# Kernel optimization log

Measured on AMD Instinct MI355X. Metric: run time of the kernel, lower is better.

The kernel has to match this reference:

```python
import jax, jax.numpy as jnp
import numpy as np

HIDDEN = 2048
NUM_Q_HEADS = 32
NUM_KV_HEADS = 8
HEAD_DIM = HIDDEN // NUM_Q_HEADS  # 64
GROUPS = NUM_Q_HEADS // NUM_KV_HEADS  # 4
MAX_WAVELENGTH = 10000.0
B, S = 2, 1024
NEG_INF = -1e9  # keras Softmax masking constant


def apply_rope(x, start_index=0, max_wavelength=MAX_WAVELENGTH):
    # x: [b, s, h, d]; keras_hub RotaryEmbedding (split-half / Llama style)
    d = x.shape[-1]
    s = x.shape[1]
    freq_range = jnp.arange(0, d, 2, dtype=jnp.float32)
    inverse_freq = 1.0 / (max_wavelength ** (freq_range / d))  # [d/2]
    positions = jnp.arange(s, dtype=jnp.float32) + start_index
    freq = positions[:, None] * inverse_freq[None, :]  # [s, d/2]
    emb = jnp.concatenate([freq, freq], axis=-1)[None, :, None, :]  # [1,s,1,d]
    cos = jnp.cos(emb).astype(x.dtype)
    sin = jnp.sin(emb).astype(x.dtype)
    x1, x2 = jnp.split(x, 2, axis=-1)
    half_rot = jnp.concatenate([-x2, x1], axis=-1)
    return x * cos + half_rot * sin


def setup_inputs() -> dict:
    key = jax.random.key(0)
    k1, k2, k3, k4, k5 = jax.random.split(key, 5)
    hidden_states = jax.random.normal(k1, (B, S, HIDDEN), dtype=jnp.float32)
    # causal mask, broadcast over batch
    attention_mask = jnp.broadcast_to(
        jnp.tril(jnp.ones((S, S), dtype=bool))[None], (B, S, S)
    )
    scale = 1.0 / np.sqrt(HIDDEN)
    Wq = jax.random.normal(k2, (HIDDEN, NUM_Q_HEADS * HEAD_DIM), dtype=jnp.float32) * scale
    Wk = jax.random.normal(k3, (HIDDEN, NUM_KV_HEADS * HEAD_DIM), dtype=jnp.float32) * scale
    Wv = jax.random.normal(k4, (HIDDEN, NUM_KV_HEADS * HEAD_DIM), dtype=jnp.float32) * scale
    Wo = jax.random.normal(k5, (NUM_Q_HEADS * HEAD_DIM, HIDDEN), dtype=jnp.float32) * scale
    return {"hidden_states": hidden_states, "attention_mask": attention_mask,
            "Wq": Wq, "Wk": Wk, "Wv": Wv, "Wo": Wo}


def reference(hidden_states, attention_mask, Wq, Wk, Wv, Wo):
    b, s, _ = hidden_states.shape
    q = (hidden_states @ Wq).reshape(b, s, NUM_Q_HEADS, HEAD_DIM)
    k = (hidden_states @ Wk).reshape(b, s, NUM_KV_HEADS, HEAD_DIM)
    v = (hidden_states @ Wv).reshape(b, s, NUM_KV_HEADS, HEAD_DIM)
    q = apply_rope(q)
    k = apply_rope(k)
    # GQA: repeat kv heads to match query heads (ops.repeat on axis 2)
    k = jnp.repeat(k, GROUPS, axis=2)
    v = jnp.repeat(v, GROUPS, axis=2)
    inv_norm = 1.0 / np.sqrt(HEAD_DIM)
    scores = jnp.einsum("bquh,bkuh->buqk", q, k) * inv_norm  # [b, h, q, k]
    scores = scores.astype(jnp.float32)
    scores = jnp.where(attention_mask[:, None, :, :], scores, NEG_INF)
    probs = jax.nn.softmax(scores, axis=-1).astype(hidden_states.dtype)
    attn = jnp.einsum("buqk,bkuh->bquh", probs, v)  # [b, q, h, hd]
    attn = attn.reshape(b, s, HIDDEN)
    return attn @ Wo
```

## Files before the change

### kernel.cpp

```cpp
#include <hip/hip_runtime.h>
#include <hip/hip_bf16.h>
#include <math.h>

#define S_LEN 1024
#define BATCH 2
#define HIDDEN 2048
#define NQH 32
#define NKVH 8
#define HD 64
#define LDQKV 3072
#define M_ROWS (BATCH * S_LEN)

typedef __attribute__((ext_vector_type(8))) short bf16x8;
typedef __attribute__((ext_vector_type(4))) float f32x4;

typedef unsigned int uint32_g __attribute__((address_space(1)));
typedef unsigned int uint32_l __attribute__((address_space(3)));

static __device__ __forceinline__ void load_lds16(const void* g, void* l) {
    __builtin_amdgcn_global_load_lds((const uint32_g*)g, (uint32_l*)l, 16, 0, 0);
}

static __device__ __forceinline__ short f2bf(float f) {
    union { __hip_bfloat16 h; short s; } cv;
    cv.h = __float2bfloat16(f);
    return cv.s;
}

__global__ __launch_bounds__(256) void conv_all_kernel(
    const float* __restrict__ X,
    const float* __restrict__ Wq, const float* __restrict__ Wk,
    const float* __restrict__ Wv, const float* __restrict__ Wo,
    short* __restrict__ Xb, short* __restrict__ Wqkvt, short* __restrict__ Wot,
    float2* __restrict__ cs2)
{
    __shared__ short Ts[64][68];
    const int tid = threadIdx.x;

    if (blockIdx.z == 4) {
        int flat = blockIdx.y * 32 + blockIdx.x;
        size_t base = (size_t)flat * 4096 + (size_t)tid * 16;
        #pragma unroll
        for (int rep = 0; rep < 2; ++rep) {
            size_t i = base + rep * 8;
            float4 a = *reinterpret_cast<const float4*>(X + i);
            float4 b = *reinterpret_cast<const float4*>(X + i + 4);
            union { bf16x8 v; short s[8]; } t;
            t.s[0] = f2bf(a.x); t.s[1] = f2bf(a.y); t.s[2] = f2bf(a.z); t.s[3] = f2bf(a.w);
            t.s[4] = f2bf(b.x); t.s[5] = f2bf(b.y); t.s[6] = f2bf(b.z); t.s[7] = f2bf(b.w);
            *reinterpret_cast<bf16x8*>(Xb + i) = t.v;
        }
        if (flat < 128) {
            int g = flat * 256 + tid;
            int s = g >> 5, i = g & 31;
            float inv_freq = 1.0f / powf(10000.0f, (float)i / 32.0f);
            float freq = (float)s * inv_freq;
            double sn, cs;
            sincos((double)freq, &sn, &cs);
            cs2[g] = make_float2((float)cs, (float)sn);
        }
        return;
    }

    const float* src; short* dst; int N;
    switch (blockIdx.z) {
        case 0: src = Wq; dst = Wqkvt;                         N = 2048; break;
        case 1: src = Wk; dst = Wqkvt + (size_t)2048 * 2048;   N = 512;  break;
        case 2: src = Wv; dst = Wqkvt + (size_t)2560 * 2048;   N = 512;  break;
        default: src = Wo; dst = Wot;                          N = 2048; break;
    }
    const int n0 = blockIdx.x * 64, k0 = blockIdx.y * 64;
    if (n0 >= N) return;

    #pragma unroll
    for (int rep = 0; rep < 4; ++rep) {
        int idx = rep * 256 + tid;
        int row = idx >> 4, c4 = (idx & 15) * 4;
        float4 v = *reinterpret_cast<const float4*>(
            src + (size_t)(k0 + row) * N + n0 + c4);
        ushort4 u;
        u.x = (unsigned short)f2bf(v.x); u.y = (unsigned short)f2bf(v.y);
        u.z = (unsigned short)f2bf(v.z); u.w = (unsigned short)f2bf(v.w);
        *reinterpret_cast<ushort4*>(&Ts[row][c4]) = u;
    }
    __syncthreads();
    #pragma unroll
    for (int rep = 0; rep < 2; ++rep) {
        int idx = rep * 256 + tid;
        int n = idx >> 3, kc = (idx & 7) * 8;
        union { bf16x8 v; short s[8]; } t;
        #pragma unroll
        for (int j = 0; j < 8; ++j) t.s[j] = Ts[kc + j][n];
        *reinterpret_cast<bf16x8*>(dst + (size_t)(n0 + n) * 2048 + k0 + kc) = t.v;
    }
}

template <bool ROPE_BF16>
__global__ __launch_bounds__(256) void gemm_bf16_kernel(
    const short* __restrict__ A, const short* __restrict__ Bt,
    float* __restrict__ C, short* __restrict__ Cb,
    short* __restrict__ vt_g,
    const float2* __restrict__ cs2, int K, int ldc)
{
    const int n0 = blockIdx.x * 64, m0 = blockIdx.y * 128;
    const int tid = threadIdx.x;
    const int w = tid >> 6, lane = tid & 63;
    const int m15 = lane & 15, q4 = lane >> 4;

    __shared__ short SL[128 * 64 + 64 * 64];
    short (*As)[64] = (short(*)[64])SL;
    short (*Bs)[64] = (short(*)[64])(SL + 128 * 64);

    f32x4 acc[2][4];
    #pragma unroll
    for (int i = 0; i < 2; ++i)
        #pragma unroll
        for (int j = 0; j < 4; ++j) acc[i][j] = (f32x4){0.f, 0.f, 0.f, 0.f};

    const int srow = lane >> 3;
    const int pchunk = lane & 7;

    for (int k0 = 0; k0 < K; k0 += 64) {
        __syncthreads();
        #pragma unroll
        for (int r = 0; r < 4; ++r) {
            int row = (w * 4 + r) * 8 + srow;
            int lchunk = pchunk ^ (row & 7);
            load_lds16(A + (size_t)(m0 + row) * K + k0 + lchunk * 8,
                       &As[(w * 4 + r) * 8][0]);
        }
        #pragma unroll
        for (int r = 0; r < 2; ++r) {
            int row = (w * 2 + r) * 8 + srow;
            int lchunk = pchunk ^ (row & 7);
            load_lds16(Bt + (size_t)(n0 + row) * K + k0 + lchunk * 8,
                       &Bs[(w * 2 + r) * 8][0]);
        }
        __syncthreads();

        #pragma unroll
        for (int ch = 0; ch < 2; ++ch) {
            bf16x8 af[2], bf[4];
            #pragma unroll
            for (int mt = 0; mt < 2; ++mt) {
                int row = w * 32 + mt * 16 + m15;
                af[mt] = *reinterpret_cast<const bf16x8*>(
                    &As[row][(((ch * 4 + q4) ^ (row & 7))) * 8]);
            }
            #pragma unroll
            for (int nt = 0; nt < 4; ++nt) {
                int row = nt * 16 + m15;
                bf[nt] = *reinterpret_cast<const bf16x8*>(
                    &Bs[row][(((ch * 4 + q4) ^ (row & 7))) * 8]);
            }
            #pragma unroll
            for (int mt = 0; mt < 2; ++mt)
                #pragma unroll
                for (int nt = 0; nt < 4; ++nt)
                    acc[mt][nt] = __builtin_amdgcn_mfma_f32_16x16x32_bf16(
                        af[mt], bf[nt], acc[mt][nt], 0, 0, 0);
        }
    }

    if (!ROPE_BF16) {
        #pragma unroll
        for (int mt = 0; mt < 2; ++mt)
            #pragma unroll
            for (int nt = 0; nt < 4; ++nt)
                #pragma unroll
                for (int reg = 0; reg < 4; ++reg)
                    C[(size_t)(m0 + w * 32 + mt * 16 + q4 * 4 + reg) * ldc
                      + n0 + nt * 16 + m15] = acc[mt][nt][reg];
    } else if (n0 < 2560) {
        #pragma unroll
        for (int mt = 0; mt < 2; ++mt) {
            #pragma unroll
            for (int reg = 0; reg < 4; ++reg) {
                int row = m0 + w * 32 + mt * 16 + q4 * 4 + reg;
                int s = row & (S_LEN - 1);
                float2 t0 = cs2[s * 32 + m15];
                float2 t1 = cs2[s * 32 + 16 + m15];
                float a0 = acc[mt][0][reg], a1 = acc[mt][1][reg];
                float a2 = acc[mt][2][reg], a3 = acc[mt][3][reg];
                size_t base = (size_t)row * ldc + n0 + m15;
                Cb[base +  0] = f2bf(a0 * t0.x - a2 * t0.y);
                Cb[base + 16] = f2bf(a1 * t1.x - a3 * t1.y);
                Cb[base + 32] = f2bf(a2 * t0.x + a0 * t0.y);
                Cb[base + 48] = f2bf(a3 * t1.x + a1 * t1.y);
            }
        }
    } else {
        __syncthreads();
        short (*VT)[136] = (short(*)[136])SL;
        #pragma unroll
        for (int mt = 0; mt < 2; ++mt) {
            #pragma unroll
            for (int nt = 0; nt < 4; ++nt) {
                ushort4 u;
                u.x = (unsigned short)f2bf(acc[mt][nt][0]);
                u.y = (unsigned short)f2bf(acc[mt][nt][1]);
                u.z = (unsigned short)f2bf(acc[mt][nt][2]);
                u.w = (unsigned short)f2bf(acc[mt][nt][3]);
                *reinterpret_cast<ushort4*>(
                    &VT[nt * 16 + m15][w * 32 + mt * 16 + q4 * 4]) = u;
            }
        }
        __syncthreads();
        const int kvh = (n0 - 2560) >> 6;
        const int b = m0 >> 10, k0loc = m0 & (S_LEN - 1);
        const int dim = tid >> 2, kc = (tid & 3) * 32;
        short* dst = vt_g + (size_t)((b * 8 + kvh) * 64 + dim) * S_LEN + k0loc + kc;
        #pragma unroll
        for (int u = 0; u < 4; ++u)
            *reinterpret_cast<bf16x8*>(dst + u * 8) =
                *reinterpret_cast<const bf16x8*>(&VT[dim][kc + u * 8]);
    }
}

__global__ __launch_bounds__(256) void attn_kernel(
    const short* __restrict__ qkvb, const short* __restrict__ vt_g,
    short* __restrict__ attn_b)
{
    const int qt = 15 - blockIdx.x;
    const int h  = blockIdx.y;
    const int b  = blockIdx.z;
    const int tid = threadIdx.x;
    const int w = tid >> 6, lane = tid & 63;
    const int kvh = h >> 2;
    const int m15 = lane & 15, q4 = lane >> 4;

    __shared__ short Ks[64][64];
    __shared__ short Vt[64][64];
    __shared__ float Ps[4][16][68];

    const int rowbase = qt * 64 + w * 16;
    const bf16x8 qf0 = *reinterpret_cast<const bf16x8*>(
        qkvb + (size_t)(b * S_LEN + rowbase + m15) * LDQKV + h * HD + q4 * 8);
    const bf16x8 qf1 = *reinterpret_cast<const bf16x8*>(
        qkvb + (size_t)(b * S_LEN + rowbase + m15) * LDQKV + h * HD + 32 + q4 * 8);

    f32x4 o4[4];
    #pragma unroll
    for (int i = 0; i < 4; ++i) o4[i] = (f32x4){0.f, 0.f, 0.f, 0.f};
    float lsum[4] = {0.f, 0.f, 0.f, 0.f};

    const int ntiles = qt + 1;
    const int r8 = lane >> 3, p8 = lane & 7;
    const int lch = (p8 ^ r8) * 8;
    const short* kbase = qkvb + (size_t)(b * S_LEN) * LDQKV + 2048 + kvh * HD;
    const short* vbase = vt_g + (size_t)(b * 8 + kvh) * 64 * S_LEN;

    for (int t = 0; t < ntiles; ++t) {
        __syncthreads();
        {
            int row0 = w * 16 + r8, row1 = w * 16 + 8 + r8;
            load_lds16(kbase + (size_t)(t * 64 + row0) * LDQKV + lch, &Ks[w * 16][0]);
            load_lds16(kbase + (size_t)(t * 64 + row1) * LDQKV + lch, &Ks[w * 16 + 8][0]);
            load_lds16(vbase + (size_t)row0 * S_LEN + t * 64 + lch, &Vt[w * 16][0]);
            load_lds16(vbase + (size_t)row1 * S_LEN + t * 64 + lch, &Vt[w * 16 + 8][0]);
        }
        __syncthreads();

        const int xr = m15 & 7;
        #pragma unroll
        for (int nt = 0; nt < 4; ++nt) {
            f32x4 acc = (f32x4){0.f, 0.f, 0.f, 0.f};
            bf16x8 kf0 = *reinterpret_cast<const bf16x8*>(
                &Ks[nt * 16 + m15][(q4 ^ xr) * 8]);
            bf16x8 kf1 = *reinterpret_cast<const bf16x8*>(
                &Ks[nt * 16 + m15][((4 + q4) ^ xr) * 8]);
            acc = __builtin_amdgcn_mfma_f32_16x16x32_bf16(qf0, kf0, acc, 0, 0, 0);
            acc = __builtin_amdgcn_mfma_f32_16x16x32_bf16(qf1, kf1, acc, 0, 0, 0);
            int colg = t * 64 + nt * 16 + m15;
            #pragma unroll
            for (int reg = 0; reg < 4; ++reg) {
                int rowg = rowbase + q4 * 4 + reg;
                float p = (colg <= rowg)
                    ? exp2f(fminf(acc[reg] * 0.180336880f, 80.f)) : 0.f;
                lsum[reg] += p;
                Ps[w][q4 * 4 + reg][nt * 16 + m15] = p;
            }
        }

        bf16x8 pf[2];
        #pragma unroll
        for (int ch = 0; ch < 2; ++ch) {
            f32x4 pa = *reinterpret_cast<const f32x4*>(&Ps[w][m15][ch * 32 + q4 * 8]);
            f32x4 pb = *reinterpret_cast<const f32x4*>(&Ps[w][m15][ch * 32 + q4 * 8 + 4]);
            union { bf16x8 v; short s[8]; } tb;
            tb.s[0] = f2bf(pa[0]); tb.s[1] = f2bf(pa[1]);
            tb.s[2] = f2bf(pa[2]); tb.s[3] = f2bf(pa[3]);
            tb.s[4] = f2bf(pb[0]); tb.s[5] = f2bf(pb[1]);
            tb.s[6] = f2bf(pb[2]); tb.s[7] = f2bf(pb[3]);
            pf[ch] = tb.v;
        }

        #pragma unroll
        for (int nt2 = 0; nt2 < 4; ++nt2) {
            bf16x8 vf0 = *reinterpret_cast<const bf16x8*>(
                &Vt[nt2 * 16 + m15][(q4 ^ xr) * 8]);
            bf16x8 vf1 = *reinterpret_cast<const bf16x8*>(
                &Vt[nt2 * 16 + m15][((4 + q4) ^ xr) * 8]);
            o4[nt2] = __builtin_amdgcn_mfma_f32_16x16x32_bf16(pf[0], vf0, o4[nt2], 0, 0, 0);
            o4[nt2] = __builtin_amdgcn_mfma_f32_16x16x32_bf16(pf[1], vf1, o4[nt2], 0, 0, 0);
        }
    }

    float invl[4];
    #pragma unroll
    for (int reg = 0; reg < 4; ++reg) {
        float l = lsum[reg];
        l += __shfl_xor(l, 1, 64);
        l += __shfl_xor(l, 2, 64);
        l += __shfl_xor(l, 4, 64);
        l += __shfl_xor(l, 8, 64);
        invl[reg] = 1.0f / l;
    }

    #pragma unroll
    for (int nt2 = 0; nt2 < 4; ++nt2)
        #pragma unroll
        for (int reg = 0; reg < 4; ++reg)
            attn_b[(size_t)(b * S_LEN + rowbase + q4 * 4 + reg) * HIDDEN
                   + h * HD + nt2 * 16 + m15] = f2bf(o4[nt2][reg] * invl[reg]);
}

extern "C" void kernel_launch(void* const* d_in, const int* in_sizes, int n_in,
                              void* d_out, int out_size, void* d_ws, size_t ws_size,
                              hipStream_t stream) {
    const float* X  = (const float*)d_in[0];
    const float* Wq = (const float*)d_in[2];
    const float* Wk = (const float*)d_in[3];
    const float* Wv = (const float*)d_in[4];
    const float* Wo = (const float*)d_in[5];
    float* out = (float*)d_out;

    short*  qkvb  = (short*)d_ws;
    short*  Xb    = qkvb + (size_t)M_ROWS * LDQKV;
    short*  Wqkvt = Xb + (size_t)HIDDEN * HIDDEN;
    short*  Wot   = Wqkvt + (size_t)LDQKV * HIDDEN;
    short*  vt_g  = Wot + (size_t)HIDDEN * HIDDEN;
    float2* cs2   = (float2*)(vt_g + (size_t)16 * 64 * S_LEN);
    short*  attn_b = Xb;

    conv_all_kernel<<<dim3(32, 32, 5), dim3(256), 0, stream>>>(
        X, Wq, Wk, Wv, Wo, Xb, Wqkvt, Wot, cs2);

    gemm_bf16_kernel<true><<<dim3(48, 16), dim3(256), 0, stream>>>(
        Xb, Wqkvt, nullptr, qkvb, vt_g, cs2, 2048, LDQKV);
    attn_kernel<<<dim3(16, 32, 2), dim3(256), 0, stream>>>(qkvb, vt_g, attn_b);
    gemm_bf16_kernel<false><<<dim3(32, 16), dim3(256), 0, stream>>>(
        attn_b, Wot, out, nullptr, nullptr, nullptr, 2048, HIDDEN);
}
```

Baseline: 214.4 us.

## Pair causal query tiles per block and double-buffer K/V tiles in attention

```diff
diff --git a/kernel.cpp b/kernel.cpp
--- a/kernel.cpp
+++ b/kernel.cpp
@@ -221,108 +221,145 @@
     const short* __restrict__ qkvb, const short* __restrict__ vt_g,
     short* __restrict__ attn_b)
 {
-    const int qt = 15 - blockIdx.x;
+    const int i  = blockIdx.x;
     const int h  = blockIdx.y;
     const int b  = blockIdx.z;
+    const int qtA = i;
+    const int qtB = 15 - i;
     const int tid = threadIdx.x;
     const int w = tid >> 6, lane = tid & 63;
     const int kvh = h >> 2;
     const int m15 = lane & 15, q4 = lane >> 4;
 
-    __shared__ short Ks[64][64];
-    __shared__ short Vt[64][64];
+    __shared__ short Ks[2][64][64];
+    __shared__ short Vt[2][64][64];
     __shared__ float Ps[4][16][68];
 
-    const int rowbase = qt * 64 + w * 16;
-    const bf16x8 qf0 = *reinterpret_cast<const bf16x8*>(
-        qkvb + (size_t)(b * S_LEN + rowbase + m15) * LDQKV + h * HD + q4 * 8);
-    const bf16x8 qf1 = *reinterpret_cast<const bf16x8*>(
-        qkvb + (size_t)(b * S_LEN + rowbase + m15) * LDQKV + h * HD + 32 + q4 * 8);
-
-    f32x4 o4[4];
-    #pragma unroll
-    for (int i = 0; i < 4; ++i) o4[i] = (f32x4){0.f, 0.f, 0.f, 0.f};
-    float lsum[4] = {0.f, 0.f, 0.f, 0.f};
-
-    const int ntiles = qt + 1;
+    const int rowbaseA = qtA * 64 + w * 16;
+    const int rowbaseB = qtB * 64 + w * 16;
+
+    const bf16x8 qfA0 = *reinterpret_cast<const bf16x8*>(
+        qkvb + (size_t)(b * S_LEN + rowbaseA + m15) * LDQKV + h * HD + q4 * 8);
+    const bf16x8 qfA1 = *reinterpret_cast<const bf16x8*>(
+        qkvb + (size_t)(b * S_LEN + rowbaseA + m15) * LDQKV + h * HD + 32 + q4 * 8);
+    const bf16x8 qfB0 = *reinterpret_cast<const bf16x8*>(
+        qkvb + (size_t)(b * S_LEN + rowbaseB + m15) * LDQKV + h * HD + q4 * 8);
+    const bf16x8 qfB1 = *reinterpret_cast<const bf16x8*>(
+        qkvb + (size_t)(b * S_LEN + rowbaseB + m15) * LDQKV + h * HD + 32 + q4 * 8);
+
+    f32x4 o4A[4], o4B[4];
+    #pragma unroll
+    for (int k = 0; k < 4; ++k) {
+        o4A[k] = (f32x4){0.f, 0.f, 0.f, 0.f};
+        o4B[k] = (f32x4){0.f, 0.f, 0.f, 0.f};
+    }
+    float lsumA[4] = {0.f, 0.f, 0.f, 0.f};
+    float lsumB[4] = {0.f, 0.f, 0.f, 0.f};
+
     const int r8 = lane >> 3, p8 = lane & 7;
     const int lch = (p8 ^ r8) * 8;
     const short* kbase = qkvb + (size_t)(b * S_LEN) * LDQKV + 2048 + kvh * HD;
     const short* vbase = vt_g + (size_t)(b * 8 + kvh) * 64 * S_LEN;
 
-    for (int t = 0; t < ntiles; ++t) {
-        __syncthreads();
-        {
-            int row0 = w * 16 + r8, row1 = w * 16 + 8 + r8;
-            load_lds16(kbase + (size_t)(t * 64 + row0) * LDQKV + lch, &Ks[w * 16][0]);
-            load_lds16(kbase + (size_t)(t * 64 + row1) * LDQKV + lch, &Ks[w * 16 + 8][0]);
-            load_lds16(vbase + (size_t)row0 * S_LEN + t * 64 + lch, &Vt[w * 16][0]);
-            load_lds16(vbase + (size_t)row1 * S_LEN + t * 64 + lch, &Vt[w * 16 + 8][0]);
-        }
-        __syncthreads();
-
-        const int xr = m15 & 7;
-        #pragma unroll
-        for (int nt = 0; nt < 4; ++nt) {
-            f32x4 acc = (f32x4){0.f, 0.f, 0.f, 0.f};
-            bf16x8 kf0 = *reinterpret_cast<const bf16x8*>(
-                &Ks[nt * 16 + m15][(q4 ^ xr) * 8]);
-            bf16x8 kf1 = *reinterpret_cast<const bf16x8*>(
-                &Ks[nt * 16 + m15][((4 + q4) ^ xr) * 8]);
-            acc = __builtin_amdgcn_mfma_f32_16x16x32_bf16(qf0, kf0, acc, 0, 0, 0);
-            acc = __builtin_amdgcn_mfma_f32_16x16x32_bf16(qf1, kf1, acc, 0, 0, 0);
-            int colg = t * 64 + nt * 16 + m15;
-            #pragma unroll
-            for (int reg = 0; reg < 4; ++reg) {
-                int rowg = rowbase + q4 * 4 + reg;
-                float p = (colg <= rowg)
-                    ? exp2f(fminf(acc[reg] * 0.180336880f, 80.f)) : 0.f;
-                lsum[reg] += p;
-                Ps[w][q4 * 4 + reg][nt * 16 + m15] = p;
-            }
-        }
-
-        bf16x8 pf[2];
-        #pragma unroll
-        for (int ch = 0; ch < 2; ++ch) {
-            f32x4 pa = *reinterpret_cast<const f32x4*>(&Ps[w][m15][ch * 32 + q4 * 8]);
-            f32x4 pb = *reinterpret_cast<const f32x4*>(&Ps[w][m15][ch * 32 + q4 * 8 + 4]);
-            union { bf16x8 v; short s[8]; } tb;
-            tb.s[0] = f2bf(pa[0]); tb.s[1] = f2bf(pa[1]);
-            tb.s[2] = f2bf(pa[2]); tb.s[3] = f2bf(pa[3]);
-            tb.s[4] = f2bf(pb[0]); tb.s[5] = f2bf(pb[1]);
-            tb.s[6] = f2bf(pb[2]); tb.s[7] = f2bf(pb[3]);
-            pf[ch] = tb.v;
-        }
-
-        #pragma unroll
-        for (int nt2 = 0; nt2 < 4; ++nt2) {
-            bf16x8 vf0 = *reinterpret_cast<const bf16x8*>(
-                &Vt[nt2 * 16 + m15][(q4 ^ xr) * 8]);
-            bf16x8 vf1 = *reinterpret_cast<const bf16x8*>(
-                &Vt[nt2 * 16 + m15][((4 + q4) ^ xr) * 8]);
-            o4[nt2] = __builtin_amdgcn_mfma_f32_16x16x32_bf16(pf[0], vf0, o4[nt2], 0, 0, 0);
-            o4[nt2] = __builtin_amdgcn_mfma_f32_16x16x32_bf16(pf[1], vf1, o4[nt2], 0, 0, 0);
-        }
-    }
-
-    float invl[4];
+#define STAGE(bf, t) do {                                                     \
+    int row0_ = w * 16 + r8, row1_ = w * 16 + 8 + r8;                         \
+    load_lds16(kbase + (size_t)((t) * 64 + row0_) * LDQKV + lch,              \
+               &Ks[bf][w * 16][0]);                                           \
+    load_lds16(kbase + (size_t)((t) * 64 + row1_) * LDQKV + lch,              \
+               &Ks[bf][w * 16 + 8][0]);                                       \
+    load_lds16(vbase + (size_t)row0_ * S_LEN + (t) * 64 + lch,                \
+               &Vt[bf][w * 16][0]);                                           \
+    load_lds16(vbase + (size_t)row1_ * S_LEN + (t) * 64 + lch,                \
+               &Vt[bf][w * 16 + 8][0]);                                       \
+} while (0)
+
+#define COMPUTE(qf0, qf1, rowbase, o4, lsum, bf, t) do {                      \
+    const int xr_ = m15 & 7;                                                  \
+    bf16x8 pf_[2];                                                            \
+    _Pragma("unroll")                                                         \
+    for (int nt = 0; nt < 4; ++nt) {                                          \
+        f32x4 acc = (f32x4){0.f, 0.f, 0.f, 0.f};                              \
+        bf16x8 kf0 = *reinterpret_cast<const bf16x8*>(                        \
+            &Ks[bf][nt * 16 + m15][(q4 ^ xr_) * 8]);                          \
+        bf16x8 kf1 = *reinterpret_cast<const bf16x8*>(                        \
+            &Ks[bf][nt * 16 + m15][((4 + q4) ^ xr_) * 8]);                    \
+        acc = __builtin_amdgcn_mfma_f32_16x16x32_bf16(qf0, kf0, acc, 0, 0, 0);\
+        acc = __builtin_amdgcn_mfma_f32_16x16x32_bf16(qf1, kf1, acc, 0, 0, 0);\
+        int colg = (t) * 64 + nt * 16 + m15;                                  \
+        _Pragma("unroll")                                                     \
+        for (int reg = 0; reg < 4; ++reg) {                                   \
+            int rowg = (rowbase) + q4 * 4 + reg;                              \
+            float p = (colg <= rowg)                                          \
+                ? exp2f(fminf(acc[reg] * 0.180336880f, 80.f)) : 0.f;          \
+            (lsum)[reg] += p;                                                 \
+            Ps[w][q4 * 4 + reg][nt * 16 + m15] = p;                           \
+        }                                                                     \
+    }                                                                         \
+    _Pragma("unroll")                                                         \
+    for (int ch = 0; ch < 2; ++ch) {                                          \
+        f32x4 pa = *reinterpret_cast<const f32x4*>(                           \
+            &Ps[w][m15][ch * 32 + q4 * 8]);                                   \
+        f32x4 pb = *reinterpret_cast<const f32x4*>(                           \
+            &Ps[w][m15][ch * 32 + q4 * 8 + 4]);                               \
+        union { bf16x8 v; short s[8]; } tb;                                   \
+        tb.s[0] = f2bf(pa[0]); tb.s[1] = f2bf(pa[1]);                         \
+        tb.s[2] = f2bf(pa[2]); tb.s[3] = f2bf(pa[3]);                         \
+        tb.s[4] = f2bf(pb[0]); tb.s[5] = f2bf(pb[1]);                         \
+        tb.s[6] = f2bf(pb[2]); tb.s[7] = f2bf(pb[3]);                         \
+        pf_[ch] = tb.v;                                                       \
+    }                                                                         \
+    _Pragma("unroll")                                                         \
+    for (int nt2 = 0; nt2 < 4; ++nt2) {                                       \
+        bf16x8 vf0 = *reinterpret_cast<const bf16x8*>(                        \
+            &Vt[bf][nt2 * 16 + m15][(q4 ^ xr_) * 8]);                         \
+        bf16x8 vf1 = *reinterpret_cast<const bf16x8*>(                        \
+            &Vt[bf][nt2 * 16 + m15][((4 + q4) ^ xr_) * 8]);                   \
+        (o4)[nt2] = __builtin_amdgcn_mfma_f32_16x16x32_bf16(                  \
+            pf_[0], vf0, (o4)[nt2], 0, 0, 0);                                 \
+        (o4)[nt2] = __builtin_amdgcn_mfma_f32_16x16x32_bf16(                  \
+            pf_[1], vf1, (o4)[nt2], 0, 0, 0);                                 \
+    }                                                                         \
+} while (0)
+
+    STAGE(0, 0);
+    __syncthreads();
+
+    for (int t = 0; t <= qtB; ++t) {
+        const int bf = t & 1;
+        if (t < qtB) STAGE(bf ^ 1, t + 1);
+        if (t <= qtA) COMPUTE(qfA0, qfA1, rowbaseA, o4A, lsumA, bf, t);
+        COMPUTE(qfB0, qfB1, rowbaseB, o4B, lsumB, bf, t);
+        __syncthreads();
+    }
+
+#undef STAGE
+#undef COMPUTE
+
+    float invlA[4], invlB[4];
     #pragma unroll
     for (int reg = 0; reg < 4; ++reg) {
-        float l = lsum[reg];
-        l += __shfl_xor(l, 1, 64);
-        l += __shfl_xor(l, 2, 64);
-        l += __shfl_xor(l, 4, 64);
-        l += __shfl_xor(l, 8, 64);
-        invl[reg] = 1.0f / l;
+        float la = lsumA[reg], lb = lsumB[reg];
+        la += __shfl_xor(la, 1, 64);
+        la += __shfl_xor(la, 2, 64);
+        la += __shfl_xor(la, 4, 64);
+        la += __shfl_xor(la, 8, 64);
+        lb += __shfl_xor(lb, 1, 64);
+        lb += __shfl_xor(lb, 2, 64);
+        lb += __shfl_xor(lb, 4, 64);
+        lb += __shfl_xor(lb, 8, 64);
+        invlA[reg] = 1.0f / la;
+        invlB[reg] = 1.0f / lb;
     }
 
     #pragma unroll
     for (int nt2 = 0; nt2 < 4; ++nt2)
         #pragma unroll
-        for (int reg = 0; reg < 4; ++reg)
-            attn_b[(size_t)(b * S_LEN + rowbase + q4 * 4 + reg) * HIDDEN
-                   + h * HD + nt2 * 16 + m15] = f2bf(o4[nt2][reg] * invl[reg]);
+        for (int reg = 0; reg < 4; ++reg) {
+            attn_b[(size_t)(b * S_LEN + rowbaseA + q4 * 4 + reg) * HIDDEN
+                   + h * HD + nt2 * 16 + m15] = f2bf(o4A[nt2][reg] * invlA[reg]);
+            attn_b[(size_t)(b * S_LEN + rowbaseB + q4 * 4 + reg) * HIDDEN
+                   + h * HD + nt2 * 16 + m15] = f2bf(o4B[nt2][reg] * invlB[reg]);
+        }
 }
 
 extern "C" void kernel_launch(void* const* d_in, const int* in_sizes, int n_in,
@@ -348,7 +385,7 @@
 
     gemm_bf16_kernel<true><<<dim3(48, 16), dim3(256), 0, stream>>>(
         Xb, Wqkvt, nullptr, qkvb, vt_g, cs2, 2048, LDQKV);
-    attn_kernel<<<dim3(16, 32, 2), dim3(256), 0, stream>>>(qkvb, vt_g, attn_b);
+    attn_kernel<<<dim3(8, 32, 2), dim3(256), 0, stream>>>(qkvb, vt_g, attn_b);
     gemm_bf16_kernel<false><<<dim3(32, 16), dim3(256), 0, stream>>>(
         attn_b, Wot, out, nullptr, nullptr, nullptr, 2048, HIDDEN);
 }
```

Result: faster. 207.5 us (-3.2%).
